# Kernel optimization log

Measured on AMD Instinct MI355X. Metric: run time of the kernel, lower is better.

The kernel has to match this reference:

```python
import jax, jax.numpy as jnp
import numpy as np

B, NA, C, NG = 32, 32768, 81, 24
POS_IOU, NEG_IOU, NPR = 0.5, 0.4, 3
VXY, VWH = 0.1, 0.2
NEG_BIG = 1e30


def cxcywh_to_xyxy(b):
    xy, wh = b[..., :2], b[..., 2:]
    return jnp.concatenate([xy - 0.5 * wh, xy + 0.5 * wh], axis=-1)


def box_iou_xyxy(a, g):
    # a: [Na,4], g: [Ng,4] -> [Na,Ng]
    lt = jnp.maximum(a[:, None, :2], g[None, :, :2])
    rb = jnp.minimum(a[:, None, 2:], g[None, :, 2:])
    wh = jnp.clip(rb - lt, 0.0)
    inter = wh[..., 0] * wh[..., 1]
    area_a = (a[:, 2] - a[:, 0]) * (a[:, 3] - a[:, 1])
    area_g = (g[:, 2] - g[:, 0]) * (g[:, 3] - g[:, 1])
    union = area_a[:, None] + area_g[None, :] - inter
    return inter / jnp.maximum(union, 1e-12)


def encode_ssd(gt, anc):
    # gt, anc: [N,4] cxcywh
    txy = (gt[:, :2] - anc[:, :2]) / anc[:, 2:] / VXY
    twh = jnp.log(gt[:, 2:] / anc[:, 2:]) / VWH
    return jnp.concatenate([txy, twh], axis=-1)


def match_one(anchors, gt_b, gt_l):
    # anchors: [Na,4], gt_b: [Ng,4], gt_l: [Ng]
    iou = box_iou_xyxy(cxcywh_to_xyxy(anchors), cxcywh_to_xyxy(gt_b))  # [Na,Ng]
    iou_max = iou.max(axis=1)
    gt_idx = jnp.argmax(iou, axis=1)          # [Na]
    best_anchor = jnp.argmax(iou, axis=0)     # [Ng]
    pos = (iou_max >= POS_IOU).at[best_anchor].set(True)
    ign = (iou_max > NEG_IOU) & ~pos
    cls_t = jnp.where(pos, gt_l[gt_idx].astype(jnp.int32), jnp.where(ign, -1, 0))
    box_t = encode_ssd(gt_b[gt_idx], anchors) * pos[:, None].astype(jnp.float32)
    return cls_t, box_t, pos


def setup_inputs() -> dict:
    key = jax.random.key(0)
    k1, k2, k3, k4, k5, k6, k7 = jax.random.split(key, 7)
    cls_pred = jax.random.normal(k1, (B, NA, C), jnp.float32)
    box_pred = jax.random.normal(k2, (B, NA, 4), jnp.float32) * 0.5
    a_xy = jax.random.uniform(k3, (NA, 2), jnp.float32)
    a_wh = jax.random.uniform(k4, (NA, 2), jnp.float32, minval=0.02, maxval=0.5)
    anchors = jnp.concatenate([a_xy, a_wh], axis=-1)
    g_xy = jax.random.uniform(k5, (B, NG, 2), jnp.float32)
    g_wh = jax.random.uniform(k6, (B, NG, 2), jnp.float32, minval=0.05, maxval=0.4)
    gt_boxes = jnp.concatenate([g_xy, g_wh], axis=-1)
    gt_labels = jax.random.randint(k7, (B, NG), 1, C, jnp.int32)
    return {"cls_pred": cls_pred, "box_pred": box_pred, "anchors": anchors,
            "gt_boxes": gt_boxes, "gt_labels": gt_labels}


def reference(cls_pred, box_pred, anchors, gt_boxes, gt_labels):
    # matching is @torch.no_grad -> constants
    cls_t, box_t, pos = jax.vmap(lambda b, l: match_one(anchors, b, l))(gt_boxes, gt_labels)
    box_t = jax.lax.stop_gradient(box_t)

    logp = jax.nn.log_softmax(cls_pred, axis=-1)
    tgt = jnp.clip(cls_t, 0)
    ce = -jnp.take_along_axis(logp, tgt[..., None], axis=-1)[..., 0]  # [B,Na]

    posf = pos.astype(jnp.float32)
    num_pos = posf.sum(-1)                       # [B]
    pos_ce_sum = (ce * posf).sum(-1)
    neg_mask = cls_t == 0
    neg_count = neg_mask.sum(-1).astype(jnp.float32)

    # descending sort of negative CE (hard-negative mining)
    neg_sorted = -jnp.sort(-jnp.where(neg_mask, ce, -NEG_BIG), axis=-1)  # [B,Na]
    ranks = jnp.arange(NA, dtype=jnp.float32)[None, :]

    num_neg = jnp.minimum(NPR * num_pos, neg_count)
    topk_sum = (neg_sorted * (ranks < num_neg[:, None])).sum(-1)
    cls_pos = jnp.where(num_neg > 0,
                        (pos_ce_sum + topk_sum) / jnp.maximum(num_pos + num_neg, 1.0),
                        pos_ce_sum / jnp.maximum(num_pos, 1.0))

    num_neg0 = jnp.minimum(100.0, neg_count)
    topk0_sum = (neg_sorted * (ranks < num_neg0[:, None])).sum(-1)
    cls_zero = jnp.where(num_neg0 > 0, topk0_sum / jnp.maximum(num_neg0, 1.0), 0.0)

    cls_loss = jnp.where(num_pos > 0, cls_pos, cls_zero)

    d = box_pred - box_t
    ad = jnp.abs(d)
    sl1 = jnp.where(ad < 1.0, 0.5 * d * d, ad - 0.5)
    reg_sum = (sl1 * posf[..., None]).sum((-1, -2))
    reg = jnp.where(num_pos > 0, reg_sum / jnp.maximum(num_pos * 4.0, 1.0), 0.0)

    return cls_loss.mean(), reg.mean(), num_pos.sum() / B
```

## Files before the change

### kernel.cpp

```cpp
#include <hip/hip_runtime.h>
#include <math.h>

#define B_  32
#define NA_ 32768
#define C_  81
#define NG_ 24

typedef const __attribute__((address_space(1))) unsigned int* gas_ptr;
typedef __attribute__((address_space(3))) unsigned int* las_ptr;

__device__ inline float wave_sum_f(float v) {
  #pragma unroll
  for (int s = 32; s >= 1; s >>= 1) v += __shfl_xor(v, s);
  return v;
}
__device__ inline unsigned long long shflx_u64(unsigned long long v, int s) {
  int lo = __shfl_xor((int)(unsigned)(v & 0xFFFFFFFFULL), s);
  int hi = __shfl_xor((int)(unsigned)(v >> 32), s);
  return ((unsigned long long)(unsigned)hi << 32) | (unsigned)lo;
}

__global__ __launch_bounds__(256) void k_match_b(
    const float* __restrict__ anchors, const float* __restrict__ gt_boxes,
    int* __restrict__ best_anchor,
    int* num_pos_g, int* notneg_g, float* pos_ce_g, float* reg_sum_g, float* out)
{
  const int g = blockIdx.x, b = blockIdx.y;
  const int tid = threadIdx.x, wave = tid >> 6, lane = tid & 63;
  if (g == 0 && b == 0) {
    if (tid < B_) { num_pos_g[tid] = 0; notneg_g[tid] = 0; pos_ce_g[tid] = 0.f; reg_sum_g[tid] = 0.f; }
    else if (tid < B_ + 3) out[tid - B_] = 0.f;
  }
  const float* gp = gt_boxes + ((size_t)b * NG_ + g) * 4;
  const float gx0 = gp[0] - 0.5f * gp[2], gy0 = gp[1] - 0.5f * gp[3];
  const float gx1 = gp[0] + 0.5f * gp[2], gy1 = gp[1] + 0.5f * gp[3];
  const float area_g = (gx1 - gx0) * (gy1 - gy0);
  unsigned long long key = 0ULL;
  #pragma unroll 4
  for (int i = 0; i < NA_ / 256; ++i) {
    const int a = i * 256 + tid;
    const float4 anc = ((const float4*)anchors)[a];
    const float ax0 = anc.x - 0.5f * anc.z, ay0 = anc.y - 0.5f * anc.w;
    const float ax1 = anc.x + 0.5f * anc.z, ay1 = anc.y + 0.5f * anc.w;
    float lx = fmaxf(ax0, gx0), ly = fmaxf(ay0, gy0);
    float rx = fminf(ax1, gx1), ry = fminf(ay1, gy1);
    float ww = fmaxf(rx - lx, 0.f), hh = fmaxf(ry - ly, 0.f);
    float inter = ww * hh;
    float uni = (ax1 - ax0) * (ay1 - ay0) + area_g - inter;
    float iou = inter / fmaxf(uni, 1e-12f);
    unsigned long long k2 =
        ((unsigned long long)__float_as_uint(iou) << 32) | (unsigned)(~(unsigned)a);
    if (k2 > key) key = k2;
  }
  #pragma unroll
  for (int s = 32; s >= 1; s >>= 1) {
    unsigned long long o = shflx_u64(key, s);
    if (o > key) key = o;
  }
  __shared__ unsigned long long red[4];
  if (lane == 0) red[wave] = key;
  __syncthreads();
  if (tid == 0) {
    unsigned long long k = red[0];
    for (int w = 1; w < 4; ++w) if (red[w] > k) k = red[w];
    best_anchor[b * NG_ + g] = (int)(~(unsigned)k);
  }
}

#define TPB 64
__global__ __launch_bounds__(64) void k_ce(
    const float* __restrict__ cls_pred, const float* __restrict__ box_pred,
    const float* __restrict__ anchors, const float* __restrict__ gt_boxes,
    const int* __restrict__ gt_labels, const int* __restrict__ best_anchor,
    int* __restrict__ neg_bits,
    int* __restrict__ num_pos_g, int* __restrict__ notneg_g,
    float* __restrict__ pos_ce_g, float* __restrict__ reg_sum_g)
{
  __shared__ float tile[TPB * C_];
  __shared__ float4 gt_xyxy[NG_];
  __shared__ float4 gt_cc[NG_];
  __shared__ float  gt_area[NG_];
  __shared__ int    label_sh[NG_];
  __shared__ int    best_a_sh[NG_];
  const int b = blockIdx.y;
  const int tid = threadIdx.x;
  const int a0 = blockIdx.x * TPB;
  const int a = a0 + tid;
  const size_t idx = (size_t)b * NA_ + a;

  if (tid < NG_) {
    const float* g = gt_boxes + ((size_t)b * NG_ + tid) * 4;
    const float cx = g[0], cy = g[1], w = g[2], h = g[3];
    const float x0 = cx - 0.5f * w, y0 = cy - 0.5f * h;
    const float x1 = cx + 0.5f * w, y1 = cy + 0.5f * h;
    gt_xyxy[tid] = make_float4(x0, y0, x1, y1);
    gt_cc[tid]   = make_float4(cx, cy, w, h);
    gt_area[tid] = (x1 - x0) * (y1 - y0);
    label_sh[tid]  = gt_labels[b * NG_ + tid];
    best_a_sh[tid] = best_anchor[b * NG_ + tid];
  }

  {
    const unsigned int* gtile =
        (const unsigned int*)(cls_pred + ((size_t)b * NA_ + a0) * C_);
    las_ptr lbase = (las_ptr)tile;
    #pragma unroll
    for (int k = 0; k < 20; ++k) {
      const int chunk = k * TPB + tid;
      __builtin_amdgcn_global_load_lds((gas_ptr)(gtile + (size_t)chunk * 4),
                                       lbase + (size_t)(k * TPB) * 4, 16, 0, 0);
    }
    if (tid < 16) {
      __builtin_amdgcn_global_load_lds((gas_ptr)(gtile + (size_t)(1280 + tid) * 4),
                                       lbase + (size_t)1280 * 4, 16, 0, 0);
    }
  }

  const float4 anc = ((const float4*)anchors)[a];
  __syncthreads();

  const float ax0 = anc.x - 0.5f * anc.z, ay0 = anc.y - 0.5f * anc.w;
  const float ax1 = anc.x + 0.5f * anc.z, ay1 = anc.y + 0.5f * anc.w;
  const float area_a = (ax1 - ax0) * (ay1 - ay0);
  float best_iou = -1.0f; int gi = 0;
  #pragma unroll 4
  for (int g = 0; g < NG_; ++g) {
    const float4 G = gt_xyxy[g];
    float lx = fmaxf(ax0, G.x), ly = fmaxf(ay0, G.y);
    float rx = fminf(ax1, G.z), ry = fminf(ay1, G.w);
    float ww = fmaxf(rx - lx, 0.f), hh = fmaxf(ry - ly, 0.f);
    float inter = ww * hh;
    float uni = area_a + gt_area[g] - inter;
    float iou = inter / fmaxf(uni, 1e-12f);
    if (iou > best_iou) { best_iou = iou; gi = g; }
  }

  bool pos = (best_iou >= 0.5f);
  #pragma unroll
  for (int g = 0; g < NG_; ++g) pos = pos || (best_a_sh[g] == a);
  const bool ign = (best_iou > 0.4f) && !pos;
  const bool neg = !pos && !ign;
  const int tgt = pos ? label_sh[gi] : 0;

  const float* row = &tile[tid * C_];
  float sum = 0.f;
  #pragma unroll 27
  for (int j = 0; j < C_; ++j) sum += __expf(row[j]);
  float ce = fmaxf(__logf(sum) - row[tgt], 0.f);

  neg_bits[idx] = neg ? __float_as_int(ce) : -1;

  float pce = 0.f, reg = 0.f;
  if (pos) {
    pce = ce;
    const float4 bp = ((const float4*)box_pred)[idx];
    const float4 G  = gt_cc[gi];
    const float tx = (G.x - anc.x) / anc.z / 0.1f;
    const float ty = (G.y - anc.y) / anc.w / 0.1f;
    const float tw = logf(G.z / anc.z) / 0.2f;
    const float th = logf(G.w / anc.w) / 0.2f;
    float d, ad;
    d = bp.x - tx; ad = fabsf(d); reg += (ad < 1.f) ? 0.5f * d * d : (ad - 0.5f);
    d = bp.y - ty; ad = fabsf(d); reg += (ad < 1.f) ? 0.5f * d * d : (ad - 0.5f);
    d = bp.z - tw; ad = fabsf(d); reg += (ad < 1.f) ? 0.5f * d * d : (ad - 0.5f);
    d = bp.w - th; ad = fabsf(d); reg += (ad < 1.f) ? 0.5f * d * d : (ad - 0.5f);
  }

  const int np_w = __popcll(__ballot(pos));
  const int nn_w = __popcll(__ballot(pos || ign));
  const float pce_w = wave_sum_f(pce);
  const float reg_w = wave_sum_f(reg);
  if (tid == 0) {
    if (np_w) atomicAdd(&num_pos_g[b], np_w);
    if (nn_w) atomicAdd(&notneg_g[b], nn_w);
    if (pce_w != 0.f) atomicAdd(&pos_ce_g[b], pce_w);
    if (reg_w != 0.f) atomicAdd(&reg_sum_g[b], reg_w);
  }
}

__global__ __launch_bounds__(1024) void k_select(
    const int* __restrict__ neg_bits,
    const int* __restrict__ num_pos_g, const int* __restrict__ notneg_g,
    const float* __restrict__ pos_ce_g, const float* __restrict__ reg_sum_g,
    float* __restrict__ out)
{
  const int b = blockIdx.x;
  const int t = threadIdx.x;
  const int wave = t >> 6, lane = t & 63;
  __shared__ unsigned cnt_sh[32];
  __shared__ float f1_sh[16], f0_sh[16];
  __shared__ unsigned cg_sh[16];
  if (t < 32) cnt_sh[t] = 0;
  int v[32];
  const int4* src4 = (const int4*)(neg_bits + (size_t)b * NA_);
  #pragma unroll
  for (int i = 0; i < 8; ++i) *(int4*)&v[4 * i] = src4[t + (i << 10)];
  const int np = num_pos_g[b];
  const int negc = NA_ - notneg_g[b];
  const int k1 = min(3 * np, negc);
  const int k0 = min(100, negc);
  __syncthreads();
  int T1 = 0, T0 = 0;
  for (int bit = 30; bit >= 0; --bit) {
    const int t1 = T1 | (1 << bit);
    const int t0 = T0 | (1 << bit);
    unsigned c = 0;
    #pragma unroll
    for (int i = 0; i < 32; ++i) {
      if (v[i] >= t1) c += (1u << 16);
      if (v[i] >= t0) c += 1u;
    }
    #pragma unroll
    for (int s = 32; s >= 1; s >>= 1) c += __shfl_xor(c, s);
    if (lane == 0) atomicAdd(&cnt_sh[bit], c);
    __syncthreads();
    const unsigned sum = cnt_sh[bit];
    if ((int)(sum >> 16) >= k1 && k1 > 0) T1 = t1;
    if ((int)(sum & 0xFFFFu) >= k0 && k0 > 0) T0 = t0;
  }
  float s1 = 0.f, s0 = 0.f; unsigned cg = 0;
  #pragma unroll
  for (int i = 0; i < 32; ++i) {
    const int x = v[i];
    if (x > T1) { s1 += __int_as_float(x); cg += (1u << 16); }
    if (x > T0) { s0 += __int_as_float(x); cg += 1u; }
  }
  #pragma unroll
  for (int s = 32; s >= 1; s >>= 1) {
    s1 += __shfl_xor(s1, s); s0 += __shfl_xor(s0, s); cg += __shfl_xor(cg, s);
  }
  if (lane == 0) { f1_sh[wave] = s1; f0_sh[wave] = s0; cg_sh[wave] = cg; }
  __syncthreads();
  if (t == 0) {
    float S1 = 0.f, S0 = 0.f; unsigned CG = 0;
    for (int w = 0; w < 16; ++w) { S1 += f1_sh[w]; S0 += f0_sh[w]; CG += cg_sh[w]; }
    const int cg1 = (int)(CG >> 16), cg0 = (int)(CG & 0xFFFFu);
    const float topk1 = (k1 > 0) ? (S1 + (float)(k1 - cg1) * __int_as_float(T1)) : 0.f;
    const float topk0 = (k0 > 0) ? (S0 + (float)(k0 - cg0) * __int_as_float(T0)) : 0.f;
    const float npf = (float)np;
    const float pce = pos_ce_g[b];
    float cls;
    if (np > 0)
      cls = (k1 > 0) ? (pce + topk1) / fmaxf(npf + (float)k1, 1.f)
                     : pce / fmaxf(npf, 1.f);
    else
      cls = (k0 > 0) ? topk0 / fmaxf((float)k0, 1.f) : 0.f;
    const float reg = (np > 0) ? reg_sum_g[b] / fmaxf(npf * 4.f, 1.f) : 0.f;
    atomicAdd(&out[0], cls * (1.0f / B_));
    atomicAdd(&out[1], reg * (1.0f / B_));
    atomicAdd(&out[2], npf * (1.0f / B_));
  }
}

extern "C" void kernel_launch(void* const* d_in, const int* in_sizes, int n_in,
                              void* d_out, int out_size, void* d_ws, size_t ws_size,
                              hipStream_t stream) {
  const float* cls_pred  = (const float*)d_in[0];
  const float* box_pred  = (const float*)d_in[1];
  const float* anchors   = (const float*)d_in[2];
  const float* gt_boxes  = (const float*)d_in[3];
  const int*   gt_labels = (const int*)d_in[4];
  float* out = (float*)d_out;

  char* ws = (char*)d_ws;
  int*   best_anchor = (int*)ws;
  int*   num_pos_g = (int*)(ws + 6144);
  int*   notneg_g  = (int*)(ws + 6144 + 128);
  float* pos_ce_g  = (float*)(ws + 6144 + 256);
  float* reg_sum_g = (float*)(ws + 6144 + 384);
  int*   neg_bits  = (int*)(ws + 8192);

  hipLaunchKernelGGL(k_match_b, dim3(NG_, B_), dim3(256), 0, stream,
                     anchors, gt_boxes, best_anchor,
                     num_pos_g, notneg_g, pos_ce_g, reg_sum_g, out);
  hipLaunchKernelGGL(k_ce, dim3(NA_ / TPB, B_), dim3(TPB), 0, stream,
                     cls_pred, box_pred, anchors, gt_boxes, gt_labels,
                     best_anchor, neg_bits,
                     num_pos_g, notneg_g, pos_ce_g, reg_sum_g);
  hipLaunchKernelGGL(k_select, dim3(B_), dim3(1024), 0, stream,
                     neg_bits, num_pos_g, notneg_g, pos_ce_g, reg_sum_g, out);
}
```

Before: 642.9 us.

## Read class logits directly from global with float4 per thread, drop LDS staging

```diff
diff --git a/kernel.cpp b/kernel.cpp
--- a/kernel.cpp
+++ b/kernel.cpp
@@ -6,10 +6,12 @@
 #define C_  81
 #define NG_ 24
 
-typedef const __attribute__((address_space(1))) unsigned int* gas_ptr;
-typedef __attribute__((address_space(3))) unsigned int* las_ptr;
-
 __device__ inline float wave_sum_f(float v) {
+  #pragma unroll
+  for (int s = 32; s >= 1; s >>= 1) v += __shfl_xor(v, s);
+  return v;
+}
+__device__ inline int wave_sum_i(int v) {
   #pragma unroll
   for (int s = 32; s >= 1; s >>= 1) v += __shfl_xor(v, s);
   return v;
@@ -67,8 +69,9 @@
   }
 }
 
-#define TPB 64
-__global__ __launch_bounds__(64) void k_ce(
+#define RPT  8
+#define TPB2 256
+__global__ __launch_bounds__(256, 2) void k_ce(
     const float* __restrict__ cls_pred, const float* __restrict__ box_pred,
     const float* __restrict__ anchors, const float* __restrict__ gt_boxes,
     const int* __restrict__ gt_labels, const int* __restrict__ best_anchor,
@@ -76,7 +79,6 @@
     int* __restrict__ num_pos_g, int* __restrict__ notneg_g,
     float* __restrict__ pos_ce_g, float* __restrict__ reg_sum_g)
 {
-  __shared__ float tile[TPB * C_];
   __shared__ float4 gt_xyxy[NG_];
   __shared__ float4 gt_cc[NG_];
   __shared__ float  gt_area[NG_];
@@ -84,9 +86,7 @@
   __shared__ int    best_a_sh[NG_];
   const int b = blockIdx.y;
   const int tid = threadIdx.x;
-  const int a0 = blockIdx.x * TPB;
-  const int a = a0 + tid;
-  const size_t idx = (size_t)b * NA_ + a;
+  const int wave = tid >> 6, lane = tid & 63;
 
   if (tid < NG_) {
     const float* g = gt_boxes + ((size_t)b * NG_ + tid) * 4;
@@ -99,78 +99,90 @@
     label_sh[tid]  = gt_labels[b * NG_ + tid];
     best_a_sh[tid] = best_anchor[b * NG_ + tid];
   }
-
-  {
-    const unsigned int* gtile =
-        (const unsigned int*)(cls_pred + ((size_t)b * NA_ + a0) * C_);
-    las_ptr lbase = (las_ptr)tile;
-    #pragma unroll
-    for (int k = 0; k < 20; ++k) {
-      const int chunk = k * TPB + tid;
-      __builtin_amdgcn_global_load_lds((gas_ptr)(gtile + (size_t)chunk * 4),
-                                       lbase + (size_t)(k * TPB) * 4, 16, 0, 0);
-    }
-    if (tid < 16) {
-      __builtin_amdgcn_global_load_lds((gas_ptr)(gtile + (size_t)(1280 + tid) * 4),
-                                       lbase + (size_t)1280 * 4, 16, 0, 0);
-    }
-  }
-
-  const float4 anc = ((const float4*)anchors)[a];
-  __syncthreads();
-
-  const float ax0 = anc.x - 0.5f * anc.z, ay0 = anc.y - 0.5f * anc.w;
-  const float ax1 = anc.x + 0.5f * anc.z, ay1 = anc.y + 0.5f * anc.w;
-  const float area_a = (ax1 - ax0) * (ay1 - ay0);
-  float best_iou = -1.0f; int gi = 0;
-  #pragma unroll 4
-  for (int g = 0; g < NG_; ++g) {
-    const float4 G = gt_xyxy[g];
-    float lx = fmaxf(ax0, G.x), ly = fmaxf(ay0, G.y);
-    float rx = fminf(ax1, G.z), ry = fminf(ay1, G.w);
-    float ww = fmaxf(rx - lx, 0.f), hh = fmaxf(ry - ly, 0.f);
-    float inter = ww * hh;
-    float uni = area_a + gt_area[g] - inter;
-    float iou = inter / fmaxf(uni, 1e-12f);
-    if (iou > best_iou) { best_iou = iou; gi = g; }
-  }
-
-  bool pos = (best_iou >= 0.5f);
-  #pragma unroll
-  for (int g = 0; g < NG_; ++g) pos = pos || (best_a_sh[g] == a);
-  const bool ign = (best_iou > 0.4f) && !pos;
-  const bool neg = !pos && !ign;
-  const int tgt = pos ? label_sh[gi] : 0;
-
-  const float* row = &tile[tid * C_];
-  float sum = 0.f;
-  #pragma unroll 27
-  for (int j = 0; j < C_; ++j) sum += __expf(row[j]);
-  float ce = fmaxf(__logf(sum) - row[tgt], 0.f);
-
-  neg_bits[idx] = neg ? __float_as_int(ce) : -1;
-
-  float pce = 0.f, reg = 0.f;
-  if (pos) {
-    pce = ce;
-    const float4 bp = ((const float4*)box_pred)[idx];
-    const float4 G  = gt_cc[gi];
-    const float tx = (G.x - anc.x) / anc.z / 0.1f;
-    const float ty = (G.y - anc.y) / anc.w / 0.1f;
-    const float tw = logf(G.z / anc.z) / 0.2f;
-    const float th = logf(G.w / anc.w) / 0.2f;
-    float d, ad;
-    d = bp.x - tx; ad = fabsf(d); reg += (ad < 1.f) ? 0.5f * d * d : (ad - 0.5f);
-    d = bp.y - ty; ad = fabsf(d); reg += (ad < 1.f) ? 0.5f * d * d : (ad - 0.5f);
-    d = bp.z - tw; ad = fabsf(d); reg += (ad < 1.f) ? 0.5f * d * d : (ad - 0.5f);
-    d = bp.w - th; ad = fabsf(d); reg += (ad < 1.f) ? 0.5f * d * d : (ad - 0.5f);
-  }
-
-  const int np_w = __popcll(__ballot(pos));
-  const int nn_w = __popcll(__ballot(pos || ign));
+  __syncthreads();
+
+  const int p = lane & 3;
+  const int base = blockIdx.x * (TPB2 * RPT) + wave * (64 * RPT);
+
+  int   npc = 0, nnc = 0;
+  float pce = 0.f, regs = 0.f;
+
+  #pragma unroll 1
+  for (int it = 0; it < RPT; ++it) {
+    const int a = base + it * 64 + lane;
+    const size_t idx = (size_t)b * NA_ + a;
+
+    const float4 anc = ((const float4*)anchors)[a];
+    const float ax0 = anc.x - 0.5f * anc.z, ay0 = anc.y - 0.5f * anc.w;
+    const float ax1 = anc.x + 0.5f * anc.z, ay1 = anc.y + 0.5f * anc.w;
+    const float area_a = (ax1 - ax0) * (ay1 - ay0);
+    float best_iou = -1.0f; int gi = 0;
+    #pragma unroll 4
+    for (int g = 0; g < NG_; ++g) {
+      const float4 G = gt_xyxy[g];
+      float lx = fmaxf(ax0, G.x), ly = fmaxf(ay0, G.y);
+      float rx = fminf(ax1, G.z), ry = fminf(ay1, G.w);
+      float ww = fmaxf(rx - lx, 0.f), hh = fmaxf(ry - ly, 0.f);
+      float inter = ww * hh;
+      float uni = area_a + gt_area[g] - inter;
+      float iou = inter / fmaxf(uni, 1e-12f);
+      if (iou > best_iou) { best_iou = iou; gi = g; }
+    }
+    bool pos = (best_iou >= 0.5f);
+    #pragma unroll
+    for (int g = 0; g < NG_; ++g) pos = pos || (best_a_sh[g] == a);
+    const bool ign = (best_iou > 0.4f) && !pos;
+    const bool neg = !pos && !ign;
+    const int tgt = pos ? label_sh[gi] : 0;
+
+    const size_t d0 = idx * 81;
+    const float4* w4 = (const float4*)(cls_pred + (d0 & ~(size_t)3));
+    float s0 = 0.f, s1 = 0.f, s2 = 0.f, s3 = 0.f;
+    #pragma unroll
+    for (int k = 0; k < 21; ++k) {
+      float4 v = w4[k];
+      if (k == 0) {
+        v.x = (p > 0) ? -1e30f : v.x;
+        v.y = (p > 1) ? -1e30f : v.y;
+        v.z = (p > 2) ? -1e30f : v.z;
+      }
+      if (k == 20) {
+        v.y = (p < 1) ? -1e30f : v.y;
+        v.z = (p < 2) ? -1e30f : v.z;
+        v.w = (p < 3) ? -1e30f : v.w;
+      }
+      s0 += __expf(v.x); s1 += __expf(v.y);
+      s2 += __expf(v.z); s3 += __expf(v.w);
+    }
+    const float sum = (s0 + s1) + (s2 + s3);
+    const float tv = cls_pred[d0 + tgt];
+    const float ce = fmaxf(__logf(sum) - tv, 0.f);
+
+    neg_bits[idx] = neg ? __float_as_int(ce) : -1;
+
+    npc += pos;
+    nnc += (pos || ign);
+    if (pos) {
+      pce += ce;
+      const float4 bp = ((const float4*)box_pred)[idx];
+      const float4 G  = gt_cc[gi];
+      const float tx = (G.x - anc.x) / anc.z / 0.1f;
+      const float ty = (G.y - anc.y) / anc.w / 0.1f;
+      const float tw = logf(G.z / anc.z) / 0.2f;
+      const float th = logf(G.w / anc.w) / 0.2f;
+      float d, ad;
+      d = bp.x - tx; ad = fabsf(d); regs += (ad < 1.f) ? 0.5f * d * d : (ad - 0.5f);
+      d = bp.y - ty; ad = fabsf(d); regs += (ad < 1.f) ? 0.5f * d * d : (ad - 0.5f);
+      d = bp.z - tw; ad = fabsf(d); regs += (ad < 1.f) ? 0.5f * d * d : (ad - 0.5f);
+      d = bp.w - th; ad = fabsf(d); regs += (ad < 1.f) ? 0.5f * d * d : (ad - 0.5f);
+    }
+  }
+
+  const int   np_w  = wave_sum_i(npc);
+  const int   nn_w  = wave_sum_i(nnc);
   const float pce_w = wave_sum_f(pce);
-  const float reg_w = wave_sum_f(reg);
-  if (tid == 0) {
+  const float reg_w = wave_sum_f(regs);
+  if (lane == 0) {
     if (np_w) atomicAdd(&num_pos_g[b], np_w);
     if (nn_w) atomicAdd(&notneg_g[b], nn_w);
     if (pce_w != 0.f) atomicAdd(&pos_ce_g[b], pce_w);
@@ -273,7 +285,7 @@
   hipLaunchKernelGGL(k_match_b, dim3(NG_, B_), dim3(256), 0, stream,
                      anchors, gt_boxes, best_anchor,
                      num_pos_g, notneg_g, pos_ce_g, reg_sum_g, out);
-  hipLaunchKernelGGL(k_ce, dim3(NA_ / TPB, B_), dim3(TPB), 0, stream,
+  hipLaunchKernelGGL(k_ce, dim3(NA_ / (TPB2 * RPT), B_), dim3(TPB2), 0, stream,
                      cls_pred, box_pred, anchors, gt_boxes, gt_labels,
                      best_anchor, neg_bits,
                      num_pos_g, notneg_g, pos_ce_g, reg_sum_g);
```

Result: faster. 609.4 us (-5.2%).
